# Kernel optimization log

Hardware: AMD Instinct MI355X
Metric: run time of the kernel (lower is better)

The kernel has to match this reference:

```python
import jax, jax.numpy as jnp
import numpy as np

jax.config.update("jax_enable_x64", True)

# config
B, S = 4, 4096
H_SIZE = 2048          # hidden_size
VOCAB = 128000         # engram_base_vocab_size
MAX_NGRAM = 3          # engram_max_ngram_size -> orders 2..3
PRIME = 500009         # engram_n_embed_per_ngram (same prime for every order)
N_HEAD = 4             # engram_n_head_per_ngram
E = 32                 # engram_embed_dim
KS = 4                 # short conv kernel size
NUM_ORDERS = MAX_NGRAM - 1
TOTAL_HEADS = NUM_ORDERS * N_HEAD
TOTAL_ROWS = PRIME * N_HEAD * NUM_ORDERS  # flat multi-head table rows


def setup_inputs() -> dict:
    key = jax.random.key(0)
    k_ids, k_h, k_tab, k_cw, k_hp, k_gp, k_op = jax.random.split(key, 7)
    input_ids = jax.random.randint(k_ids, (B, S), 0, VOCAB, dtype=jnp.int64)
    hidden_states = jax.random.normal(k_h, (B, S, H_SIZE), dtype=jnp.float32)
    # identity compressed-tokenizer mapping buffer
    mapping = jnp.arange(VOCAB, dtype=jnp.int64)
    # deterministic odd multipliers, seeded like _build_multipliers
    rng = np.random.default_rng(0 * 10007 + 0 * 1009)
    mults = rng.integers(1, 2 ** 31, size=(NUM_ORDERS, N_HEAD, MAX_NGRAM))
    multipliers = jnp.asarray(mults * 2 + 1, dtype=jnp.int64)
    table = 0.02 * jax.random.normal(k_tab, (TOTAL_ROWS, E), dtype=jnp.float32)
    conv_w = 0.1 * jax.random.normal(k_cw, (E, KS), dtype=jnp.float32)  # depthwise taps
    conv_b = jnp.zeros((E,), dtype=jnp.float32)
    Wh = 0.05 * jax.random.normal(k_hp, (E, TOTAL_HEADS * E), dtype=jnp.float32)
    Wg = 0.02 * jax.random.normal(k_gp, (E, H_SIZE), dtype=jnp.float32)
    Wo = 0.02 * jax.random.normal(k_op, (H_SIZE, E), dtype=jnp.float32)
    return {"input_ids": input_ids, "hidden_states": hidden_states,
            "mapping": mapping, "multipliers": multipliers, "table": table,
            "conv_w": conv_w, "conv_b": conv_b, "Wh": Wh, "Wg": Wg, "Wo": Wo}


def _hash_indices(compressed, multipliers):
    """XOR-mix n-gram hash indices -> [B, S, TOTAL_HEADS] int64."""
    all_idx = []
    offset = 0
    for oi, k in enumerate(range(2, MAX_NGRAM + 1)):
        # forward sliding window, clamped at last token (matches cat/expand trick)
        pos = jnp.minimum(jnp.arange(S)[:, None] + jnp.arange(k)[None, :], S - 1)  # [S,k]
        ng = compressed[:, pos]                                  # [B,S,k]
        m = multipliers[oi, :, :k]                               # [nh,k]
        prod = ng[:, :, None, :] * m[None, None, :, :]           # [B,S,nh,k]
        h = prod[..., 0]
        for p in range(1, k):
            h = h ^ prod[..., p]
        idx = h % PRIME + (offset + jnp.arange(N_HEAD, dtype=jnp.int64) * PRIME)
        all_idx.append(idx)
        offset += PRIME * N_HEAD
    return jnp.concatenate(all_idx, axis=-1)


def reference(input_ids, hidden_states, mapping, multipliers, table,
              conv_w, conv_b, Wh, Wg, Wo):
    compressed = mapping[input_ids]                              # [B,S]
    indices = _hash_indices(compressed, multipliers)             # [B,S,TOTAL_HEADS]
    emb = table[indices].reshape(B, S, TOTAL_HEADS * E)          # multi-head gather
    emb = emb @ Wh.T                                             # head_proj -> [B,S,E]
    # causal depthwise short conv (kernel KS, left pad KS-1)
    xp = jnp.pad(emb, ((0, 0), (KS - 1, 0), (0, 0)))
    emb = sum(xp[:, j:j + S, :] * conv_w[:, j] for j in range(KS)) + conv_b
    gate = jax.nn.sigmoid(hidden_states @ Wg.T)                  # [B,S,E]
    return (gate * emb) @ Wo.T                                   # [B,S,H_SIZE]
```

## Files before the change

### kernel.cpp

```cpp
#include <hip/hip_runtime.h>
#include <hip/hip_bf16.h>
#include <stdint.h>

#define HSZ 2048
#define PRIME 500009u
#define CHUNK 64
#define NCH 32

typedef __attribute__((ext_vector_type(8))) short short8;
typedef __attribute__((ext_vector_type(4))) float f32x4;
typedef __attribute__((ext_vector_type(4))) unsigned uint4v;
typedef __attribute__((ext_vector_type(2))) unsigned uint2v;

#define MEMFENCE asm volatile("" ::: "memory")
#define BARRIER() do { MEMFENCE; __builtin_amdgcn_s_barrier(); MEMFENCE; } while (0)
#define WAIT_LGKM0 asm volatile("s_waitcnt lgkmcnt(0)" ::: "memory")
#define WAIT_VM(n) asm volatile("s_waitcnt vmcnt(" #n ")" ::: "memory")

__device__ __forceinline__ unsigned pk2(float x, float y) {
  __hip_bfloat162 h = __float22bfloat162_rn(make_float2(x, y));
  return *reinterpret_cast<unsigned*>(&h);
}
__device__ __forceinline__ short f2bf(float f) {
  __hip_bfloat16 h = __float2bfloat16(f);
  return *reinterpret_cast<short*>(&h);
}
__device__ __forceinline__ short8 pack8(float4 a, float4 b) {
  uint4v u = {pk2(a.x, a.y), pk2(a.z, a.w), pk2(b.x, b.y), pk2(b.z, b.w)};
  return __builtin_bit_cast(short8, u);
}
__device__ __forceinline__ short8 load8_bf(const float* __restrict__ p) {
  float4 a = *reinterpret_cast<const float4*>(p);
  float4 b = *reinterpret_cast<const float4*>(p + 4);
  return pack8(a, b);
}
__device__ __forceinline__ void gload_lds16(const float* g, void* l) {
  __builtin_amdgcn_global_load_lds(
      (const __attribute__((address_space(1))) void*)g,
      (__attribute__((address_space(3))) void*)l, 16, 0, 0);
}

__global__ __launch_bounds__(256, 2) void engram_fused(
    const int* __restrict__ ids, const int* __restrict__ mapping,
    const unsigned* __restrict__ mult, const float* __restrict__ table,
    const float* __restrict__ Wh, const float* __restrict__ hidden,
    const float* __restrict__ cw, const float* __restrict__ cb,
    const float* __restrict__ Wg, const float* __restrict__ Wo,
    float* __restrict__ out) {
  __shared__ __align__(16) float hbuf[2][32][CHUNK];
  __shared__ __align__(16) short A_lds[48][264];
  __shared__ __align__(16) float emb48[48][36];
  __shared__ float emb_c[32][33];
  __shared__ __align__(16) short ge_lds[32][40];
  __shared__ int idx_lds[384];

  const int tid = threadIdx.x;
  const int wid = tid >> 6, lane = tid & 63;
  const int l16 = lane & 15, q = lane >> 4;
  const int t0 = blockIdx.x * 32;

  auto STAGE = [&](int buf, int kc) {
#pragma unroll
    for (int j = 0; j < 2; ++j) {
      int r = wid * 8 + j * 4 + (lane >> 4);
      unsigned c4 = (((unsigned)l16 * 16u) ^ (((unsigned)r & 7u) << 4)) >> 2;
      const float* src = hidden + (size_t)(t0 + r) * HSZ + kc * CHUNK + c4;
      gload_lds16(src, &hbuf[buf][wid * 8 + j * 4][0]);
    }
  };

  STAGE(0, 0);
  STAGE(1, 1);

#pragma unroll
  for (int p = 0; p < 2; ++p) {
    int hh = p * 256 + tid;
    if (hh < 384) {
      int slot = hh >> 3, head = hh & 7;
      int tg = t0 - 16 + slot;
      if (tg < 0) tg = 0;
      int b = tg >> 12, s = tg & 4095;
      const int* idb = ids + (b << 12);
      int s1 = s + 1 > 4095 ? 4095 : s + 1;
      int s2 = s + 2 > 4095 ? 4095 : s + 2;
      uint64_t c0 = (unsigned)mapping[idb[s]];
      uint64_t c1 = (unsigned)mapping[idb[s1]];
      uint64_t c2 = (unsigned)mapping[idb[s2]];
      int mb = head * 3;
      uint64_t h = (c0 * (uint64_t)mult[mb]) ^ (c1 * (uint64_t)mult[mb + 1]);
      if (head >= 4) h ^= c2 * (uint64_t)mult[mb + 2];
      idx_lds[hh] = (int)((unsigned)(h % PRIME) + (unsigned)head * PRIME);
    }
  }
  WAIT_LGKM0; BARRIER();

#pragma unroll
  for (int p = 0; p < 12; ++p) {
    int r = p * 32 + (tid >> 3);
    int c4 = (tid & 7) * 4;
    int row = idx_lds[r];
    float4 v = *reinterpret_cast<const float4*>(table + (size_t)row * 32 + c4);
    uint2v pk = {pk2(v.x, v.y), pk2(v.z, v.w)};
    *reinterpret_cast<uint2v*>(&A_lds[r >> 3][(r & 7) * 32 + c4]) = pk;
  }
  WAIT_LGKM0; BARRIER();

  for (int job = wid; job < 6; job += 4) {
    int jt = job >> 1, e0 = (job & 1) * 16;
    f32x4 acc = {0.f, 0.f, 0.f, 0.f};
#pragma unroll
    for (int ks = 0; ks < 8; ++ks) {
      short8 wf = load8_bf(Wh + (size_t)(e0 + l16) * 256 + ks * 32 + q * 8);
      short8 a = *reinterpret_cast<const short8*>(&A_lds[jt * 16 + l16][ks * 32 + q * 8]);
      acc = __builtin_amdgcn_mfma_f32_16x16x32_bf16(wf, a, acc, 0, 0, 0);
    }
    *reinterpret_cast<f32x4*>(&emb48[jt * 16 + l16][e0 + q * 4]) = acc;
  }
  WAIT_LGKM0; BARRIER();

#pragma unroll
  for (int it = 0; it < 4; ++it) {
    int ii = it * 256 + tid;
    int tl = ii >> 5, e = ii & 31;
    int s = (t0 & 4095) + tl;
    float a = cb[e];
#pragma unroll
    for (int j = 0; j < 4; ++j)
      if (s - 3 + j >= 0) a += cw[e * 4 + j] * emb48[13 + tl + j][e];
    emb_c[tl][e] = a;
  }
  WAIT_LGKM0; BARRIER();

  const int tt = wid >> 1, ee = wid & 1;
  const int R = tt * 16 + l16;
  const unsigned sw = ((unsigned)R & 7u) << 4;
  const char* hb0 = (const char*)&hbuf[0][R][0];
  const char* hb1 = (const char*)&hbuf[1][R][0];
  const float* wgp = Wg + (size_t)(ee * 16 + l16) * HSZ + q * 8;
  f32x4 acc = {0.f, 0.f, 0.f, 0.f};

  for (int kc = 0; kc < NCH - 1; ++kc) {
    WAIT_VM(8);
    BARRIER();
    const char* hb = (kc & 1) ? hb1 : hb0;
    unsigned x0 = q * 32u;
    float4 a0 = *reinterpret_cast<const float4*>(hb + (x0 ^ sw));
    float4 a1 = *reinterpret_cast<const float4*>(hb + ((x0 + 16) ^ sw));
    float4 a2 = *reinterpret_cast<const float4*>(hb + ((x0 + 128) ^ sw));
    float4 a3 = *reinterpret_cast<const float4*>(hb + ((x0 + 144) ^ sw));
    short8 A0 = pack8(a0, a1);
    short8 A1 = pack8(a2, a3);
    short8 B0 = load8_bf(wgp + kc * CHUNK);
    short8 B1 = load8_bf(wgp + kc * CHUNK + 32);
    WAIT_LGKM0;
    BARRIER();
    if (kc < NCH - 2) STAGE(kc & 1, kc + 2);
    acc = __builtin_amdgcn_mfma_f32_16x16x32_bf16(A0, B0, acc, 0, 0, 0);
    acc = __builtin_amdgcn_mfma_f32_16x16x32_bf16(A1, B1, acc, 0, 0, 0);
  }
  {
    WAIT_VM(0);
    BARRIER();
    unsigned x0 = q * 32u;
    float4 a0 = *reinterpret_cast<const float4*>(hb1 + (x0 ^ sw));
    float4 a1 = *reinterpret_cast<const float4*>(hb1 + ((x0 + 16) ^ sw));
    float4 a2 = *reinterpret_cast<const float4*>(hb1 + ((x0 + 128) ^ sw));
    float4 a3 = *reinterpret_cast<const float4*>(hb1 + ((x0 + 144) ^ sw));
    short8 B0 = load8_bf(wgp + (NCH - 1) * CHUNK);
    short8 B1 = load8_bf(wgp + (NCH - 1) * CHUNK + 32);
    acc = __builtin_amdgcn_mfma_f32_16x16x32_bf16(pack8(a0, a1), B0, acc, 0, 0, 0);
    acc = __builtin_amdgcn_mfma_f32_16x16x32_bf16(pack8(a2, a3), B1, acc, 0, 0, 0);
  }

#pragma unroll
  for (int j = 0; j < 4; ++j) {
    int r = tt * 16 + q * 4 + j, c = ee * 16 + l16;
    float g = 1.f / (1.f + __expf(-acc[j]));
    ge_lds[r][c] = f2bf(g * emb_c[r][c]);
  }
  WAIT_LGKM0; BARRIER();

  short8 Af0 = *reinterpret_cast<const short8*>(&ge_lds[l16][q * 8]);
  short8 Af1 = *reinterpret_cast<const short8*>(&ge_lds[16 + l16][q * 8]);
  float* orow0 = out + (size_t)(t0 + l16) * HSZ;
  float* orow1 = out + (size_t)(t0 + 16 + l16) * HSZ;
  int hbase = wid * 512;
  for (int ht = 0; ht < 32; ++ht) {
    int h0 = hbase + ht * 16;
    short8 aw = load8_bf(Wo + (size_t)(h0 + l16) * 32 + q * 8);
    f32x4 z = {0.f, 0.f, 0.f, 0.f};
    f32x4 o0 = __builtin_amdgcn_mfma_f32_16x16x32_bf16(aw, Af0, z, 0, 0, 0);
    f32x4 o1 = __builtin_amdgcn_mfma_f32_16x16x32_bf16(aw, Af1, z, 0, 0, 0);
    *reinterpret_cast<f32x4*>(orow0 + h0 + q * 4) = o0;
    *reinterpret_cast<f32x4*>(orow1 + h0 + q * 4) = o1;
  }
}

extern "C" void kernel_launch(void* const* d_in, const int* in_sizes, int n_in,
                              void* d_out, int out_size, void* d_ws, size_t ws_size,
                              hipStream_t stream) {
  const int* ids = (const int*)d_in[0];
  const float* hidden = (const float*)d_in[1];
  const int* mapping = (const int*)d_in[2];
  const unsigned* mult = (const unsigned*)d_in[3];
  const float* table = (const float*)d_in[4];
  const float* cw = (const float*)d_in[5];
  const float* cb = (const float*)d_in[6];
  const float* Wh = (const float*)d_in[7];
  const float* Wg = (const float*)d_in[8];
  const float* Wo = (const float*)d_in[9];
  float* out = (float*)d_out;

  engram_fused<<<512, 256, 0, stream>>>(ids, mapping, mult, table, Wh, hidden,
                                        cw, cb, Wg, Wo, out);
}
```

Measured before the change: 79.03 us.

## Halve tokens per block and split gate GEMM K-dimension across wave pairs

Each block now handles 16 tokens instead of 32, so the grid doubles to 1024 blocks, and launch bounds ask for 3 blocks per CU. The hidden-state chunk grows to 128 columns with half as many iterations. The gate GEMM is split over K between wave pairs, and the partial sums are combined through LDS before the sigmoid. The goal is more parallelism and better latency hiding in this memory-bound kernel. The cost is a larger recomputed halo fraction for the conv window and gather, plus an extra reduction barrier.

```diff
diff --git a/kernel.cpp b/kernel.cpp
--- a/kernel.cpp
+++ b/kernel.cpp
@@ -4,8 +4,8 @@
 
 #define HSZ 2048
 #define PRIME 500009u
-#define CHUNK 64
-#define NCH 32
+#define CHUNK 128
+#define NCH 16
 
 typedef __attribute__((ext_vector_type(8))) short short8;
 typedef __attribute__((ext_vector_type(4))) float f32x4;
@@ -40,62 +40,60 @@
       (__attribute__((address_space(3))) void*)l, 16, 0, 0);
 }
 
-__global__ __launch_bounds__(256, 2) void engram_fused(
+__global__ __launch_bounds__(256, 3) void engram_fused(
     const int* __restrict__ ids, const int* __restrict__ mapping,
     const unsigned* __restrict__ mult, const float* __restrict__ table,
     const float* __restrict__ Wh, const float* __restrict__ hidden,
     const float* __restrict__ cw, const float* __restrict__ cb,
     const float* __restrict__ Wg, const float* __restrict__ Wo,
     float* __restrict__ out) {
-  __shared__ __align__(16) float hbuf[2][32][CHUNK];
-  __shared__ __align__(16) short A_lds[48][264];
-  __shared__ __align__(16) float emb48[48][36];
-  __shared__ float emb_c[32][33];
-  __shared__ __align__(16) short ge_lds[32][40];
-  __shared__ int idx_lds[384];
+  __shared__ __align__(16) float hbuf[2][16][CHUNK];
+  __shared__ __align__(16) short A_lds[32][264];
+  __shared__ __align__(16) float emb32[32][36];
+  __shared__ float emb_c[16][33];
+  __shared__ __align__(16) short ge_lds[16][40];
+  __shared__ float accred[2][4][64];
+  __shared__ int idx_lds[256];
 
   const int tid = threadIdx.x;
   const int wid = tid >> 6, lane = tid & 63;
   const int l16 = lane & 15, q = lane >> 4;
-  const int t0 = blockIdx.x * 32;
+  const int t0 = blockIdx.x * 16;
 
   auto STAGE = [&](int buf, int kc) {
 #pragma unroll
     for (int j = 0; j < 2; ++j) {
-      int r = wid * 8 + j * 4 + (lane >> 4);
-      unsigned c4 = (((unsigned)l16 * 16u) ^ (((unsigned)r & 7u) << 4)) >> 2;
-      const float* src = hidden + (size_t)(t0 + r) * HSZ + kc * CHUNK + c4;
-      gload_lds16(src, &hbuf[buf][wid * 8 + j * 4][0]);
+      int r0 = wid * 4 + j * 2;
+      int r = r0 + (lane >> 5);
+      unsigned cf = (((unsigned)(lane & 31) * 16u) ^ (((unsigned)r & 7u) << 4)) >> 2;
+      const float* src = hidden + (size_t)(t0 + r) * HSZ + kc * CHUNK + cf;
+      gload_lds16(src, &hbuf[buf][r0][0]);
     }
   };
 
   STAGE(0, 0);
   STAGE(1, 1);
 
-#pragma unroll
-  for (int p = 0; p < 2; ++p) {
-    int hh = p * 256 + tid;
-    if (hh < 384) {
-      int slot = hh >> 3, head = hh & 7;
-      int tg = t0 - 16 + slot;
-      if (tg < 0) tg = 0;
-      int b = tg >> 12, s = tg & 4095;
-      const int* idb = ids + (b << 12);
-      int s1 = s + 1 > 4095 ? 4095 : s + 1;
-      int s2 = s + 2 > 4095 ? 4095 : s + 2;
-      uint64_t c0 = (unsigned)mapping[idb[s]];
-      uint64_t c1 = (unsigned)mapping[idb[s1]];
-      uint64_t c2 = (unsigned)mapping[idb[s2]];
-      int mb = head * 3;
-      uint64_t h = (c0 * (uint64_t)mult[mb]) ^ (c1 * (uint64_t)mult[mb + 1]);
-      if (head >= 4) h ^= c2 * (uint64_t)mult[mb + 2];
-      idx_lds[hh] = (int)((unsigned)(h % PRIME) + (unsigned)head * PRIME);
-    }
-  }
-  WAIT_LGKM0; BARRIER();
-
-#pragma unroll
-  for (int p = 0; p < 12; ++p) {
+  {
+    int slot = tid >> 3, head = tid & 7;
+    int tg = t0 - 16 + slot;
+    if (tg < 0) tg = 0;
+    int b = tg >> 12, s = tg & 4095;
+    const int* idb = ids + (b << 12);
+    int s1 = s + 1 > 4095 ? 4095 : s + 1;
+    int s2 = s + 2 > 4095 ? 4095 : s + 2;
+    uint64_t c0 = (unsigned)mapping[idb[s]];
+    uint64_t c1 = (unsigned)mapping[idb[s1]];
+    uint64_t c2 = (unsigned)mapping[idb[s2]];
+    int mb = head * 3;
+    uint64_t h = (c0 * (uint64_t)mult[mb]) ^ (c1 * (uint64_t)mult[mb + 1]);
+    if (head >= 4) h ^= c2 * (uint64_t)mult[mb + 2];
+    idx_lds[tid] = (int)((unsigned)(h % PRIME) + (unsigned)head * PRIME);
+  }
+  WAIT_LGKM0; BARRIER();
+
+#pragma unroll
+  for (int p = 0; p < 8; ++p) {
     int r = p * 32 + (tid >> 3);
     int c4 = (tid & 7) * 4;
     int row = idx_lds[r];
@@ -105,8 +103,8 @@
   }
   WAIT_LGKM0; BARRIER();
 
-  for (int job = wid; job < 6; job += 4) {
-    int jt = job >> 1, e0 = (job & 1) * 16;
+  {
+    int jt = wid >> 1, e0 = (wid & 1) * 16;
     f32x4 acc = {0.f, 0.f, 0.f, 0.f};
 #pragma unroll
     for (int ks = 0; ks < 8; ++ks) {
@@ -114,36 +112,35 @@
       short8 a = *reinterpret_cast<const short8*>(&A_lds[jt * 16 + l16][ks * 32 + q * 8]);
       acc = __builtin_amdgcn_mfma_f32_16x16x32_bf16(wf, a, acc, 0, 0, 0);
     }
-    *reinterpret_cast<f32x4*>(&emb48[jt * 16 + l16][e0 + q * 4]) = acc;
-  }
-  WAIT_LGKM0; BARRIER();
-
-#pragma unroll
-  for (int it = 0; it < 4; ++it) {
+    *reinterpret_cast<f32x4*>(&emb32[jt * 16 + l16][e0 + q * 4]) = acc;
+  }
+  WAIT_LGKM0; BARRIER();
+
+#pragma unroll
+  for (int it = 0; it < 2; ++it) {
     int ii = it * 256 + tid;
     int tl = ii >> 5, e = ii & 31;
     int s = (t0 & 4095) + tl;
     float a = cb[e];
 #pragma unroll
     for (int j = 0; j < 4; ++j)
-      if (s - 3 + j >= 0) a += cw[e * 4 + j] * emb48[13 + tl + j][e];
+      if (s - 3 + j >= 0) a += cw[e * 4 + j] * emb32[13 + tl + j][e];
     emb_c[tl][e] = a;
   }
   WAIT_LGKM0; BARRIER();
 
-  const int tt = wid >> 1, ee = wid & 1;
-  const int R = tt * 16 + l16;
-  const unsigned sw = ((unsigned)R & 7u) << 4;
-  const char* hb0 = (const char*)&hbuf[0][R][0];
-  const char* hb1 = (const char*)&hbuf[1][R][0];
-  const float* wgp = Wg + (size_t)(ee * 16 + l16) * HSZ + q * 8;
+  const int ee = wid & 1, kh = wid >> 1;
+  const unsigned sw = ((unsigned)l16 & 7u) << 4;
+  const char* hb0 = (const char*)&hbuf[0][0][0] + l16 * 512;
+  const char* hb1 = (const char*)&hbuf[1][0][0] + l16 * 512;
+  const float* wgp = Wg + (size_t)(ee * 16 + l16) * HSZ + kh * 64 + q * 8;
+  const unsigned x0 = (unsigned)(kh * 256 + q * 32);
   f32x4 acc = {0.f, 0.f, 0.f, 0.f};
 
   for (int kc = 0; kc < NCH - 1; ++kc) {
     WAIT_VM(8);
     BARRIER();
     const char* hb = (kc & 1) ? hb1 : hb0;
-    unsigned x0 = q * 32u;
     float4 a0 = *reinterpret_cast<const float4*>(hb + (x0 ^ sw));
     float4 a1 = *reinterpret_cast<const float4*>(hb + ((x0 + 16) ^ sw));
     float4 a2 = *reinterpret_cast<const float4*>(hb + ((x0 + 128) ^ sw));
@@ -161,7 +158,6 @@
   {
     WAIT_VM(0);
     BARRIER();
-    unsigned x0 = q * 32u;
     float4 a0 = *reinterpret_cast<const float4*>(hb1 + (x0 ^ sw));
     float4 a1 = *reinterpret_cast<const float4*>(hb1 + ((x0 + 16) ^ sw));
     float4 a2 = *reinterpret_cast<const float4*>(hb1 + ((x0 + 128) ^ sw));
@@ -172,27 +168,31 @@
     acc = __builtin_amdgcn_mfma_f32_16x16x32_bf16(pack8(a2, a3), B1, acc, 0, 0, 0);
   }
 
-#pragma unroll
-  for (int j = 0; j < 4; ++j) {
-    int r = tt * 16 + q * 4 + j, c = ee * 16 + l16;
-    float g = 1.f / (1.f + __expf(-acc[j]));
-    ge_lds[r][c] = f2bf(g * emb_c[r][c]);
-  }
-  WAIT_LGKM0; BARRIER();
-
-  short8 Af0 = *reinterpret_cast<const short8*>(&ge_lds[l16][q * 8]);
-  short8 Af1 = *reinterpret_cast<const short8*>(&ge_lds[16 + l16][q * 8]);
-  float* orow0 = out + (size_t)(t0 + l16) * HSZ;
-  float* orow1 = out + (size_t)(t0 + 16 + l16) * HSZ;
-  int hbase = wid * 512;
+  if (kh == 1) {
+#pragma unroll
+    for (int j = 0; j < 4; ++j) accred[ee][j][lane] = acc[j];
+  }
+  WAIT_LGKM0; BARRIER();
+  if (kh == 0) {
+#pragma unroll
+    for (int j = 0; j < 4; ++j) {
+      float s = acc[j] + accred[ee][j][lane];
+      int r = q * 4 + j, c = ee * 16 + l16;
+      float g = 1.f / (1.f + __expf(-s));
+      ge_lds[r][c] = f2bf(g * emb_c[r][c]);
+    }
+  }
+  WAIT_LGKM0; BARRIER();
+
+  short8 Af = *reinterpret_cast<const short8*>(&ge_lds[l16][q * 8]);
+  float* orow = out + (size_t)(t0 + l16) * HSZ;
+#pragma unroll 4
   for (int ht = 0; ht < 32; ++ht) {
-    int h0 = hbase + ht * 16;
+    int h0 = wid * 512 + ht * 16;
     short8 aw = load8_bf(Wo + (size_t)(h0 + l16) * 32 + q * 8);
     f32x4 z = {0.f, 0.f, 0.f, 0.f};
-    f32x4 o0 = __builtin_amdgcn_mfma_f32_16x16x32_bf16(aw, Af0, z, 0, 0, 0);
-    f32x4 o1 = __builtin_amdgcn_mfma_f32_16x16x32_bf16(aw, Af1, z, 0, 0, 0);
-    *reinterpret_cast<f32x4*>(orow0 + h0 + q * 4) = o0;
-    *reinterpret_cast<f32x4*>(orow1 + h0 + q * 4) = o1;
+    f32x4 o = __builtin_amdgcn_mfma_f32_16x16x32_bf16(aw, Af, z, 0, 0, 0);
+    *reinterpret_cast<f32x4*>(orow + h0 + q * 4) = o;
   }
 }
 
@@ -211,6 +211,6 @@
   const float* Wo = (const float*)d_in[9];
   float* out = (float*)d_out;
 
-  engram_fused<<<512, 256, 0, stream>>>(ids, mapping, mult, table, Wh, hidden,
-                                        cw, cb, Wg, Wo, out);
-}
+  engram_fused<<<1024, 256, 0, stream>>>(ids, mapping, mult, table, Wh, hidden,
+                                         cw, cb, Wg, Wo, out);
+}
```

Result: slower. 101.9 us (+29.0%).
